# Kernel optimization log

Hardware: AMD Instinct MI355X
Metric: run time of the kernel (lower is better)

## Reference

```python
import jax, jax.numpy as jnp
import numpy as np

D_MODEL = 256
D_INNER = 512   # expand=2
D_STATE = 16
D_CONV = 4
DT_RANK = 16    # ceil(256/16)
N_LAYERS = 4
CITY = 300
BATCH = 32
EPS = 1e-5


def setup_inputs() -> dict:
    key = jax.random.key(0)
    ks = jax.random.split(key, 12)
    def rn(k, shape, scale=0.02):
        return (jax.random.normal(k, shape) * scale).astype(jnp.float32)
    inp = {}
    inp["coords"]   = jax.random.uniform(ks[0], (BATCH, CITY, 2), jnp.float32)
    inp["emb_W"]    = rn(ks[1], (D_MODEL, 2), 0.5)
    inp["emb_b"]    = jnp.zeros((D_MODEL,), jnp.float32)
    inp["ln_w"]     = jnp.ones((N_LAYERS, D_MODEL), jnp.float32)
    inp["ln_b"]     = jnp.zeros((N_LAYERS, D_MODEL), jnp.float32)
    inp["in_W"]     = rn(ks[2], (N_LAYERS, 2 * D_INNER, D_MODEL))
    inp["conv_W"]   = rn(ks[3], (N_LAYERS, D_INNER, D_CONV), 0.1)
    inp["conv_b"]   = jnp.zeros((N_LAYERS, D_INNER), jnp.float32)
    inp["xproj_W"]  = rn(ks[4], (N_LAYERS, DT_RANK + 2 * D_STATE, D_INNER))
    inp["dtproj_W"] = rn(ks[5], (N_LAYERS, D_INNER, DT_RANK), 0.1)
    inp["dtproj_b"] = rn(ks[6], (N_LAYERS, D_INNER), 0.1)
    # A initialized like mamba: S4D-real, A = -exp(A_log) with A in [1, 16]
    inp["A_log"]    = jnp.log(1.0 + jax.random.uniform(ks[7], (N_LAYERS, D_INNER, D_STATE), jnp.float32) * 15.0)
    inp["D_skip"]   = jnp.ones((N_LAYERS, D_INNER), jnp.float32)
    inp["out_W"]    = rn(ks[8], (N_LAYERS, D_MODEL, D_INNER))
    inp["normf_w"]  = jnp.ones((D_MODEL,), jnp.float32)
    inp["normf_b"]  = jnp.zeros((D_MODEL,), jnp.float32)
    inp["head_W"]   = rn(ks[9], (CITY, D_MODEL))
    return inp


def _layernorm(x, w, b):
    m = jnp.mean(x, axis=-1, keepdims=True)
    v = jnp.mean(jnp.square(x - m), axis=-1, keepdims=True)
    return (x - m) * jax.lax.rsqrt(v + EPS) * w + b


def _mamba_mixer(x, in_W, conv_W, conv_b, xproj_W, dtproj_W, dtproj_b, A_log, D_skip, out_W):
    # x: (B, L, d_model)
    Bsz = x.shape[0]
    xz = jnp.einsum('bld,ed->ble', x, in_W)            # (B, L, 2*d_inner)
    xi, z = jnp.split(xz, 2, axis=-1)                   # each (B, L, d_inner)
    # causal depthwise conv1d along L
    xc = jnp.swapaxes(xi, 1, 2)                         # (B, d_inner, L)
    xc = jax.lax.conv_general_dilated(
        xc, conv_W[:, None, :], (1,), [(D_CONV - 1, 0)],
        feature_group_count=D_INNER, dimension_numbers=('NCH', 'OIH', 'NCH'))
    xc = jax.nn.silu(jnp.swapaxes(xc, 1, 2) + conv_b)   # (B, L, d_inner)
    dbl = jnp.einsum('bld,ed->ble', xc, xproj_W)        # (B, L, dt_rank + 2*d_state)
    dt, Bm, Cm = jnp.split(dbl, [DT_RANK, DT_RANK + D_STATE], axis=-1)
    dt = jax.nn.softplus(jnp.einsum('blr,dr->bld', dt, dtproj_W) + dtproj_b)  # (B, L, d_inner)
    A = -jnp.exp(A_log)                                 # (d_inner, d_state)

    def step(h, inp):
        x_t, dt_t, B_t, C_t = inp                       # (B,dI),(B,dI),(B,dS),(B,dS)
        dA = jnp.exp(dt_t[..., None] * A)               # (B, dI, dS)
        h = dA * h + (dt_t * x_t)[..., None] * B_t[:, None, :]
        y = jnp.einsum('bds,bs->bd', h, C_t)
        return h, y

    h0 = jnp.zeros((Bsz, D_INNER, D_STATE), x.dtype)
    xs = (jnp.swapaxes(xc, 0, 1), jnp.swapaxes(dt, 0, 1),
          jnp.swapaxes(Bm, 0, 1), jnp.swapaxes(Cm, 0, 1))
    _, ys = jax.lax.scan(step, h0, xs)                  # ys: (L, B, d_inner)
    y = jnp.swapaxes(ys, 0, 1) + xc * D_skip
    y = y * jax.nn.silu(z)
    return jnp.einsum('ble,de->bld', y, out_W)          # (B, L, d_model)


def reference(coords, emb_W, emb_b, ln_w, ln_b, in_W, conv_W, conv_b, xproj_W,
              dtproj_W, dtproj_b, A_log, D_skip, out_W, normf_w, normf_b, head_W):
    x = jnp.einsum('blc,dc->bld', coords, emb_W) + emb_b
    residual = None
    for i in range(N_LAYERS):
        residual = x if residual is None else x + residual
        h = _layernorm(residual, ln_w[i], ln_b[i])
        x = _mamba_mixer(h, in_W[i], conv_W[i], conv_b[i], xproj_W[i],
                         dtproj_W[i], dtproj_b[i], A_log[i], D_skip[i], out_W[i])
    res = x + residual
    # final fused add + RMSNorm (is_rms_norm=True with LayerNorm weight/bias)
    rms = res * jax.lax.rsqrt(jnp.mean(res * res, axis=-1, keepdims=True) + EPS)
    out = rms * normf_w + normf_b
    logits = jnp.einsum('bld,cd->blc', out, head_W)     # (B, L, city_count)
    return logits
```

## Files before the change

kernel.cpp:

```cpp
#include <hip/hip_runtime.h>
#include <hip/hip_bf16.h>
#include <math.h>

#define D_MODEL 256
#define D_INNER 512
#define D_STATE 16
#define D_CONV 4
#define DT_RANK 16
#define N_LAYERS 4
#define CITY 300
#define BATCH 32
#define SEQ 300
#define NTOK (BATCH * SEQ)
#define NSEG 15
#define SEGLEN (SEQ / NSEG)

typedef __attribute__((ext_vector_type(8))) short short8v;
typedef __attribute__((ext_vector_type(4))) float f32x4;
typedef __attribute__((ext_vector_type(2))) float f32x2;

#define L2E_F 1.44269504088896340736f
#define LN2_F 0.69314718055994530942f

__device__ __forceinline__ float fexp2(float x) { return __builtin_amdgcn_exp2f(x); }
__device__ __forceinline__ float flog2(float x) { return __builtin_amdgcn_logf(x); }

__device__ __forceinline__ float fast_sig(float x) {
    return __builtin_amdgcn_rcpf(1.f + fexp2(-x * L2E_F));
}

__device__ __forceinline__ float softplus_f(float x) {
    float t = fexp2(-fabsf(x) * L2E_F);
    return fmaxf(x, 0.f) + flog2(1.f + t) * LN2_F;
}

__device__ __forceinline__ unsigned short f2b(float a) {
    __hip_bfloat16 h = __float2bfloat16(a);
    return *reinterpret_cast<unsigned short*>(&h);
}

__device__ __forceinline__ float b2f(unsigned short u) {
    unsigned int x = ((unsigned int)u) << 16;
    return __uint_as_float(x);
}

__device__ __forceinline__ float dtproj8(const float* rb, const f32x2* w2, float dtbv) {
    const f32x2* r2 = (const f32x2*)rb;
    f32x2 a0, a1, a2, a3;
    a0.x = dtbv; a0.y = 0.f;
    a1.x = 0.f; a1.y = 0.f;
    a2 = a1; a3 = a1;
    a0 = __builtin_elementwise_fma(r2[0], w2[0], a0);
    a1 = __builtin_elementwise_fma(r2[1], w2[1], a1);
    a2 = __builtin_elementwise_fma(r2[2], w2[2], a2);
    a3 = __builtin_elementwise_fma(r2[3], w2[3], a3);
    a0 = __builtin_elementwise_fma(r2[4], w2[4], a0);
    a1 = __builtin_elementwise_fma(r2[5], w2[5], a1);
    a2 = __builtin_elementwise_fma(r2[6], w2[6], a2);
    a3 = __builtin_elementwise_fma(r2[7], w2[7], a3);
    f32x2 s = (a0 + a1) + (a2 + a3);
    return s.x + s.y;
}

__global__ void cvt4_kernel(const float* __restrict__ s0, unsigned short* __restrict__ d0, int n0,
                            const float* __restrict__ s1, unsigned short* __restrict__ d1, int n1,
                            const float* __restrict__ s2, unsigned short* __restrict__ d2, int n2,
                            const float* __restrict__ s3, unsigned short* __restrict__ d3, int n3) {
    int stride = gridDim.x * blockDim.x;
    int tid = blockIdx.x * blockDim.x + threadIdx.x;
    for (int i = tid; i < n0 / 4; i += stride) {
        float4 v = ((const float4*)s0)[i];
        ushort4 o; o.x = f2b(v.x); o.y = f2b(v.y); o.z = f2b(v.z); o.w = f2b(v.w);
        ((ushort4*)d0)[i] = o;
    }
    for (int i = tid; i < n1 / 4; i += stride) {
        float4 v = ((const float4*)s1)[i];
        ushort4 o; o.x = f2b(v.x); o.y = f2b(v.y); o.z = f2b(v.z); o.w = f2b(v.w);
        ((ushort4*)d1)[i] = o;
    }
    for (int i = tid; i < n2 / 4; i += stride) {
        float4 v = ((const float4*)s2)[i];
        ushort4 o; o.x = f2b(v.x); o.y = f2b(v.y); o.z = f2b(v.z); o.w = f2b(v.w);
        ((ushort4*)d2)[i] = o;
    }
    for (int i = tid; i < n3 / 4; i += stride) {
        float4 v = ((const float4*)s3)[i];
        ushort4 o; o.x = f2b(v.x); o.y = f2b(v.y); o.z = f2b(v.z); o.w = f2b(v.w);
        ((ushort4*)d3)[i] = o;
    }
}

__global__ void embed_ln_kernel(const float* __restrict__ coords,
                                const float* __restrict__ eW,
                                const float* __restrict__ eb,
                                const float* __restrict__ w,
                                const float* __restrict__ b,
                                float* __restrict__ resid,
                                unsigned short* __restrict__ hb) {
    int t = blockIdx.x, d = threadIdx.x;
    float c0 = coords[t * 2 + 0];
    float c1 = coords[t * 2 + 1];
    float r = c0 * eW[d * 2 + 0] + c1 * eW[d * 2 + 1] + eb[d];
    resid[t * D_MODEL + d] = r;
    float s1 = r, s2 = r * r;
#pragma unroll
    for (int m = 1; m < 64; m <<= 1) {
        s1 += __shfl_xor(s1, m);
        s2 += __shfl_xor(s2, m);
    }
    __shared__ float p1[4], p2[4];
    if ((d & 63) == 0) { p1[d >> 6] = s1; p2[d >> 6] = s2; }
    __syncthreads();
    s1 = (p1[0] + p1[1]) + (p1[2] + p1[3]);
    s2 = (p2[0] + p2[1]) + (p2[2] + p2[3]);
    float mean = s1 * (1.f / D_MODEL);
    float var = s2 * (1.f / D_MODEL) - mean * mean;
    hb[t * D_MODEL + d] = f2b((r - mean) * rsqrtf(var + 1e-5f) * w[d] + b[d]);
}

template <int BM, int BN, bool GN, bool OB>
__global__ __launch_bounds__(256, 2) void gemm_mfma(const unsigned short* __restrict__ A,
                                                    const unsigned short* __restrict__ W,
                                                    void* __restrict__ C, int N, int K) {
    constexpr int TI = BM / 32;
    constexpr int TJ = BN / 32;
    __shared__ short Als[BM * 32];
    __shared__ short Bls[BN * 32];
    const int tid = threadIdx.x;
    const int lane = tid & 63, wid = tid >> 6;
    const int wr = wid >> 1, wc = wid & 1;
    const int t0 = blockIdx.x * BM, n0 = blockIdx.y * BN;
    f32x4 acc[TI][TJ] = {};

    for (int k0 = 0; k0 < K; k0 += 32) {
#pragma unroll
        for (int it = 0; it < BM / 64; ++it) {
            int s = tid + it * 256;
            int m = s >> 2, q = s & 3;
            uint4 p = *(const uint4*)(A + (size_t)(t0 + m) * K + k0 + q * 8);
            *(uint4*)&Als[(((m >> 4) * 4 + q) * 16 + (m & 15)) * 8] = p;
        }
#pragma unroll
        for (int it = 0; it < BN / 64; ++it) {
            int s = tid + it * 256;
            int n = s >> 2, q = s & 3;
            int nrow = n0 + n;
            uint4 p = make_uint4(0u, 0u, 0u, 0u);
            if (!GN || nrow < N)
                p = *(const uint4*)(W + (size_t)nrow * K + k0 + q * 8);
            *(uint4*)&Bls[(((n >> 4) * 4 + q) * 16 + (n & 15)) * 8] = p;
        }
        __syncthreads();
        short8v af[TI], bf[TJ];
#pragma unroll
        for (int i = 0; i < TI; i++)
            af[i] = *(const short8v*)&Als[(wr * TI + i) * 512 + lane * 8];
#pragma unroll
        for (int j = 0; j < TJ; j++)
            bf[j] = *(const short8v*)&Bls[(wc * TJ + j) * 512 + lane * 8];
#pragma unroll
        for (int i = 0; i < TI; i++)
#pragma unroll
            for (int j = 0; j < TJ; j++)
                acc[i][j] = __builtin_amdgcn_mfma_f32_16x16x32_bf16(
                    af[i], bf[j], acc[i][j], 0, 0, 0);
        __syncthreads();
    }
    const int rq = lane >> 4, cn = lane & 15;
#pragma unroll
    for (int i = 0; i < TI; i++) {
        int trow = t0 + wr * (BM / 2) + i * 16 + rq * 4;
#pragma unroll
        for (int j = 0; j < TJ; j++) {
            int ncol = n0 + wc * (BN / 2) + j * 16 + cn;
            if (!GN || ncol < N) {
#pragma unroll
                for (int reg = 0; reg < 4; reg++) {
                    if constexpr (OB)
                        ((unsigned short*)C)[(size_t)(trow + reg) * N + ncol] =
                            f2b(acc[i][j][reg]);
                    else
                        ((float*)C)[(size_t)(trow + reg) * N + ncol] = acc[i][j][reg];
                }
            }
        }
    }
}

template <bool RMS>
__global__ __launch_bounds__(256, 2) void gemm_out_ln(const unsigned short* __restrict__ A,
                                                      const unsigned short* __restrict__ W,
                                                      float* __restrict__ resid,
                                                      const float* __restrict__ w,
                                                      const float* __restrict__ b,
                                                      unsigned short* __restrict__ hb) {
    constexpr int TI = 2, TJ = 8;
    const int K = D_INNER;
    __shared__ short Als[64 * 32];
    __shared__ short Bls[256 * 32];
    __shared__ float rs1[2][64], rs2[2][64];
    const int tid = threadIdx.x;
    const int lane = tid & 63, wid = tid >> 6;
    const int wr = wid >> 1, wc = wid & 1;
    const int t0 = blockIdx.x * 64;
    f32x4 acc[TI][TJ] = {};

    for (int k0 = 0; k0 < K; k0 += 32) {
        {
            int s = tid;
            int m = s >> 2, q = s & 3;
            uint4 p = *(const uint4*)(A + (size_t)(t0 + m) * K + k0 + q * 8);
            *(uint4*)&Als[(((m >> 4) * 4 + q) * 16 + (m & 15)) * 8] = p;
        }
#pragma unroll
        for (int it = 0; it < 4; ++it) {
            int s = tid + it * 256;
            int n = s >> 2, q = s & 3;
            uint4 p = *(const uint4*)(W + (size_t)n * K + k0 + q * 8);
            *(uint4*)&Bls[(((n >> 4) * 4 + q) * 16 + (n & 15)) * 8] = p;
        }
        __syncthreads();
        short8v af[TI], bf[TJ];
#pragma unroll
        for (int i = 0; i < TI; i++)
            af[i] = *(const short8v*)&Als[(wr * TI + i) * 512 + lane * 8];
#pragma unroll
        for (int j = 0; j < TJ; j++)
            bf[j] = *(const short8v*)&Bls[(wc * TJ + j) * 512 + lane * 8];
#pragma unroll
        for (int i = 0; i < TI; i++)
#pragma unroll
            for (int j = 0; j < TJ; j++)
                acc[i][j] = __builtin_amdgcn_mfma_f32_16x16x32_bf16(
                    af[i], bf[j], acc[i][j], 0, 0, 0);
        __syncthreads();
    }
    const int rq = lane >> 4, cn = lane & 15;
    float s1p[TI][4], s2p[TI][4];
#pragma unroll
    for (int i = 0; i < TI; i++) {
        int trow = t0 + wr * 32 + i * 16 + rq * 4;
#pragma unroll
        for (int reg = 0; reg < 4; reg++) { s1p[i][reg] = 0.f; s2p[i][reg] = 0.f; }
#pragma unroll
        for (int j = 0; j < TJ; j++) {
            int c = wc * 128 + j * 16 + cn;
#pragma unroll
            for (int reg = 0; reg < 4; reg++) {
                float rv = acc[i][j][reg] + resid[(size_t)(trow + reg) * D_MODEL + c];
                acc[i][j][reg] = rv;
                s1p[i][reg] += rv;
                s2p[i][reg] = fmaf(rv, rv, s2p[i][reg]);
            }
        }
    }
#pragma unroll
    for (int m = 1; m < 16; m <<= 1) {
#pragma unroll
        for (int i = 0; i < TI; i++)
#pragma unroll
            for (int reg = 0; reg < 4; reg++) {
                s1p[i][reg] += __shfl_xor(s1p[i][reg], m);
                s2p[i][reg] += __shfl_xor(s2p[i][reg], m);
            }
    }
    if (cn == 0) {
#pragma unroll
        for (int i = 0; i < TI; i++)
#pragma unroll
            for (int reg = 0; reg < 4; reg++) {
                int rloc = wr * 32 + i * 16 + rq * 4 + reg;
                rs1[wc][rloc] = s1p[i][reg];
                rs2[wc][rloc] = s2p[i][reg];
            }
    }
    __syncthreads();
    float wv[TJ], bv[TJ];
#pragma unroll
    for (int j = 0; j < TJ; j++) {
        int c = wc * 128 + j * 16 + cn;
        wv[j] = w[c];
        bv[j] = b[c];
    }
#pragma unroll
    for (int i = 0; i < TI; i++) {
        int trow = t0 + wr * 32 + i * 16 + rq * 4;
#pragma unroll
        for (int reg = 0; reg < 4; reg++) {
            int rloc = wr * 32 + i * 16 + rq * 4 + reg;
            float S1 = rs1[0][rloc] + rs1[1][rloc];
            float S2 = rs2[0][rloc] + rs2[1][rloc];
            float mean, rstd;
            if constexpr (RMS) {
                mean = 0.f;
                rstd = rsqrtf(S2 * (1.f / D_MODEL) + 1e-5f);
            } else {
                mean = S1 * (1.f / D_MODEL);
                float var = S2 * (1.f / D_MODEL) - mean * mean;
                rstd = rsqrtf(var + 1e-5f);
            }
#pragma unroll
            for (int j = 0; j < TJ; j++) {
                int c = wc * 128 + j * 16 + cn;
                float rv = acc[i][j][reg];
                hb[(size_t)(trow + reg) * D_MODEL + c] =
                    f2b((rv - mean) * rstd * wv[j] + bv[j]);
                if constexpr (!RMS)
                    resid[(size_t)(trow + reg) * D_MODEL + c] = rv;
            }
        }
    }
}

__global__ void conv_silu_kernel(const unsigned short* __restrict__ xzb,
                                 const float* __restrict__ cW,
                                 const float* __restrict__ cb,
                                 unsigned short* __restrict__ xcb) {
    int idx = blockIdx.x * blockDim.x + threadIdx.x;
    int d4 = (idx & 127) * 4;
    int t = idx >> 7;
    int l = t % SEQ;
    float4 acc = *(const float4*)(cb + d4);
    float4 wA = *(const float4*)(cW + (d4 + 0) * 4);
    float4 wB = *(const float4*)(cW + (d4 + 1) * 4);
    float4 wC = *(const float4*)(cW + (d4 + 2) * 4);
    float4 wD = *(const float4*)(cW + (d4 + 3) * 4);
#pragma unroll
    for (int k = 0; k < D_CONV; k++) {
        int ll = l - 3 + k;
        if (ll >= 0) {
            ushort4 u = *(const ushort4*)(xzb + (size_t)(t - 3 + k) * 1024 + d4);
            float wa = (k == 0) ? wA.x : (k == 1) ? wA.y : (k == 2) ? wA.z : wA.w;
            float wb = (k == 0) ? wB.x : (k == 1) ? wB.y : (k == 2) ? wB.z : wB.w;
            float wc = (k == 0) ? wC.x : (k == 1) ? wC.y : (k == 2) ? wC.z : wC.w;
            float wd = (k == 0) ? wD.x : (k == 1) ? wD.y : (k == 2) ? wD.z : wD.w;
            acc.x = fmaf(b2f(u.x), wa, acc.x);
            acc.y = fmaf(b2f(u.y), wb, acc.y);
            acc.z = fmaf(b2f(u.z), wc, acc.z);
            acc.w = fmaf(b2f(u.w), wd, acc.w);
        }
    }
    ushort4 ob;
    ob.x = f2b(acc.x * fast_sig(acc.x));
    ob.y = f2b(acc.y * fast_sig(acc.y));
    ob.z = f2b(acc.z * fast_sig(acc.z));
    ob.w = f2b(acc.w * fast_sig(acc.w));
    *(ushort4*)(xcb + (size_t)t * 512 + d4) = ob;
}

__global__ __launch_bounds__(960) void scan_block(
    const unsigned short* __restrict__ xcb, const float* __restrict__ dbl,
    const unsigned short* __restrict__ xzb,
    const float* __restrict__ A_log, const float* __restrict__ Dskip,
    const float* __restrict__ dtW, const float* __restrict__ dtb,
    float* __restrict__ dts, unsigned short* __restrict__ yb) {
    __shared__ float lh[NSEG * D_STATE * 64];
    __shared__ float lsd[NSEG * 64];
    const int b = blockIdx.x, dg = blockIdx.y;
    const int tid = threadIdx.x;
    const int lane = tid & 63;
    const int seg = __builtin_amdgcn_readfirstlane(tid >> 6);
    const int d = (dg << 6) + lane;
    f32x2 A2[8], w2[8];
#pragma unroll
    for (int s4 = 0; s4 < 4; s4++) {
        float4 v = *(const float4*)(A_log + (size_t)d * D_STATE + s4 * 4);
        f32x2 pa, pb;
        pa.x = -fexp2(v.x * L2E_F) * L2E_F;
        pa.y = -fexp2(v.y * L2E_F) * L2E_F;
        pb.x = -fexp2(v.z * L2E_F) * L2E_F;
        pb.y = -fexp2(v.w * L2E_F) * L2E_F;
        A2[s4 * 2 + 0] = pa;
        A2[s4 * 2 + 1] = pb;
        float4 w = *(const float4*)(dtW + (size_t)d * DT_RANK + s4 * 4);
        f32x2 qa, qb;
        qa.x = w.x; qa.y = w.y;
        qb.x = w.z; qb.y = w.w;
        w2[s4 * 2 + 0] = qa;
        w2[s4 * 2 + 1] = qb;
    }
    const float dtbv = dtb[d], dsk = Dskip[d];
    const size_t tb = (size_t)b * SEQ + (size_t)seg * SEGLEN;
    const float* __restrict__ dr = dbl + tb * 48;
    const unsigned short* __restrict__ xp = xcb + tb * 512 + d;
    const unsigned short* __restrict__ zp = xzb + tb * 1024 + 512 + d;
    float* __restrict__ dtp = dts + tb * 512 + d;
    unsigned short* __restrict__ yp = yb + tb * 512 + d;

    {
        f32x2 h2[8];
#pragma unroll
        for (int i = 0; i < 8; i++) { h2[i].x = 0.f; h2[i].y = 0.f; }
        float sdt = 0.f;
        float dbA[32], dbB[32];
#pragma unroll
        for (int i = 0; i < 8; i++) ((float4*)dbA)[i] = ((const float4*)dr)[i];
        float xv = b2f(xp[0]);
        for (int l = 0; l < SEGLEN; l += 2) {
            const float4* nr1 = (const float4*)(dr + (size_t)(l + 1) * 48);
#pragma unroll
            for (int i = 0; i < 8; i++) ((float4*)dbB)[i] = nr1[i];
            float xv1 = b2f(xp[(size_t)(l + 1) * 512]);
            {
                float acc = dtproj8(dbA, w2, dtbv);
                float dtt = softplus_f(acc);
                dtp[(size_t)l * 512] = dtt;
                sdt += dtt;
                float dtx = dtt * xv;
                f32x2 dtt2, dtx2;
                dtt2.x = dtt; dtt2.y = dtt;
                dtx2.x = dtx; dtx2.y = dtx;
                const f32x2* B2 = (const f32x2*)(dbA + 16);
#pragma unroll
                for (int i = 0; i < 8; i++) {
                    f32x2 g = dtt2 * A2[i];
                    f32x2 e;
                    e.x = fexp2(g.x);
                    e.y = fexp2(g.y);
                    h2[i] = __builtin_elementwise_fma(e, h2[i], dtx2 * B2[i]);
                }
            }
            const float4* nr2 = (const float4*)(dr + (size_t)(l + 2) * 48);
#pragma unroll
            for (int i = 0; i < 8; i++) ((float4*)dbA)[i] = nr2[i];
            float xv2 = b2f(xp[(size_t)(l + 2) * 512]);
            if (l + 1 < SEGLEN) {
                float acc = dtproj8(dbB, w2, dtbv);
                float dtt = softplus_f(acc);
                dtp[(size_t)(l + 1) * 512] = dtt;
                sdt += dtt;
                float dtx = dtt * xv1;
                f32x2 dtt2, dtx2;
                dtt2.x = dtt; dtt2.y = dtt;
                dtx2.x = dtx; dtx2.y = dtx;
                const f32x2* B2 = (const f32x2*)(dbB + 16);
#pragma unroll
                for (int i = 0; i < 8; i++) {
                    f32x2 g = dtt2 * A2[i];
                    f32x2 e;
                    e.x = fexp2(g.x);
                    e.y = fexp2(g.y);
                    h2[i] = __builtin_elementwise_fma(e, h2[i], dtx2 * B2[i]);
                }
            }
            xv = xv2;
        }
#pragma unroll
        for (int i = 0; i < 8; i++) {
            lh[(seg * D_STATE + 2 * i + 0) * 64 + lane] = h2[i].x;
            lh[(seg * D_STATE + 2 * i + 1) * 64 + lane] = h2[i].y;
        }
        lsd[seg * 64 + lane] = sdt;
    }
    __syncthreads();
    for (int it = tid; it < D_STATE * 64; it += 960) {
        int ch = it & 63, s = it >> 6;
        float As2 = -fexp2(A_log[(size_t)((dg << 6) + ch) * D_STATE + s] * L2E_F) * L2E_F;
        float hl[NSEG], sd[NSEG];
#pragma unroll
        for (int sg = 0; sg < NSEG; sg++) {
            hl[sg] = lh[(sg * D_STATE + s) * 64 + ch];
            sd[sg] = lsd[sg * 64 + ch];
        }
        float H = 0.f;
#pragma unroll
        for (int sg = 0; sg < NSEG; sg++) {
            lh[(sg * D_STATE + s) * 64 + ch] = H;
            H = fmaf(fexp2(As2 * sd[sg]), H, hl[sg]);
        }
    }
    __syncthreads();
    {
        f32x2 h2[8];
#pragma unroll
        for (int i = 0; i < 8; i++) {
            h2[i].x = lh[(seg * D_STATE + 2 * i + 0) * 64 + lane];
            h2[i].y = lh[(seg * D_STATE + 2 * i + 1) * 64 + lane];
        }
        float dbA[32], dbB[32];
#pragma unroll
        for (int i = 0; i < 8; i++) ((float4*)dbA)[i] = ((const float4*)(dr + 16))[i];
        float xv = b2f(xp[0]), zv = b2f(zp[0]);
        float dt0 = dtp[0];
        for (int l = 0; l < SEGLEN; l += 2) {
            const float4* nr1 = (const float4*)(dr + (size_t)(l + 1) * 48 + 16);
#pragma unroll
            for (int i = 0; i < 8; i++) ((float4*)dbB)[i] = nr1[i];
            float xv1 = b2f(xp[(size_t)(l + 1) * 512]);
            float zv1 = b2f(zp[(size_t)(l + 1) * 1024]);
            float dt1 = dtp[(size_t)(l + 1) * 512];
            {
                float dtt = dt0;
                float dtx = dtt * xv;
                f32x2 dtt2, dtx2;
                dtt2.x = dtt; dtt2.y = dtt;
                dtx2.x = dtx; dtx2.y = dtx;
                f32x2 ya, yc;
                ya.x = 0.f; ya.y = 0.f; yc = ya;
                const f32x2* B2 = (const f32x2*)dbA;
                const f32x2* C2 = (const f32x2*)(dbA + 16);
#pragma unroll
                for (int i = 0; i < 8; i++) {
                    f32x2 g = dtt2 * A2[i];
                    f32x2 e;
                    e.x = fexp2(g.x);
                    e.y = fexp2(g.y);
                    h2[i] = __builtin_elementwise_fma(e, h2[i], dtx2 * B2[i]);
                    if (i & 1)
                        yc = __builtin_elementwise_fma(h2[i], C2[i], yc);
                    else
                        ya = __builtin_elementwise_fma(h2[i], C2[i], ya);
                }
                f32x2 ys = ya + yc;
                float y = ys.x + ys.y;
                yp[(size_t)l * 512] = f2b((y + xv * dsk) * (zv * fast_sig(zv)));
            }
            const float4* nr2 = (const float4*)(dr + (size_t)(l + 2) * 48 + 16);
#pragma unroll
            for (int i = 0; i < 8; i++) ((float4*)dbA)[i] = nr2[i];
            float xv2 = b2f(xp[(size_t)(l + 2) * 512]);
            float zv2 = b2f(zp[(size_t)(l + 2) * 1024]);
            float dt2 = dtp[(size_t)(l + 2) * 512];
            if (l + 1 < SEGLEN) {
                float dtt = dt1;
                float dtx = dtt * xv1;
                f32x2 dtt2, dtx2;
                dtt2.x = dtt; dtt2.y = dtt;
                dtx2.x = dtx; dtx2.y = dtx;
                f32x2 ya, yc;
                ya.x = 0.f; ya.y = 0.f; yc = ya;
                const f32x2* B2 = (const f32x2*)dbB;
                const f32x2* C2 = (const f32x2*)(dbB + 16);
#pragma unroll
                for (int i = 0; i < 8; i++) {
                    f32x2 g = dtt2 * A2[i];
                    f32x2 e;
                    e.x = fexp2(g.x);
                    e.y = fexp2(g.y);
                    h2[i] = __builtin_elementwise_fma(e, h2[i], dtx2 * B2[i]);
                    if (i & 1)
                        yc = __builtin_elementwise_fma(h2[i], C2[i], yc);
                    else
                        ya = __builtin_elementwise_fma(h2[i], C2[i], ya);
                }
                f32x2 ys = ya + yc;
                float y = ys.x + ys.y;
                yp[(size_t)(l + 1) * 512] = f2b((y + xv1 * dsk) * (zv1 * fast_sig(zv1)));
            }
            xv = xv2; zv = zv2; dt0 = dt2;
        }
    }
}

extern "C" void kernel_launch(void* const* d_in, const int* in_sizes, int n_in,
                              void* d_out, int out_size, void* d_ws, size_t ws_size,
                              hipStream_t stream) {
    const float* coords   = (const float*)d_in[0];
    const float* emb_W    = (const float*)d_in[1];
    const float* emb_b    = (const float*)d_in[2];
    const float* ln_w     = (const float*)d_in[3];
    const float* ln_b     = (const float*)d_in[4];
    const float* in_W     = (const float*)d_in[5];
    const float* conv_W   = (const float*)d_in[6];
    const float* conv_b   = (const float*)d_in[7];
    const float* xproj_W  = (const float*)d_in[8];
    const float* dtproj_W = (const float*)d_in[9];
    const float* dtproj_b = (const float*)d_in[10];
    const float* A_log    = (const float*)d_in[11];
    const float* D_skip   = (const float*)d_in[12];
    const float* out_W    = (const float*)d_in[13];
    const float* normf_w  = (const float*)d_in[14];
    const float* normf_b  = (const float*)d_in[15];
    const float* head_W   = (const float*)d_in[16];
    float* out = (float*)d_out;

    const int T = NTOK;
    float* resid = (float*)d_ws;
    float* dbl   = resid + (size_t)T * D_MODEL;
    float* dts   = dbl + (size_t)T * 48;
    unsigned short* hb     = (unsigned short*)(dts + (size_t)T * D_INNER);
    unsigned short* xzb    = hb + (size_t)T * D_MODEL;
    unsigned short* xcb    = xzb + (size_t)T * 2 * D_INNER;
    unsigned short* yb     = xcb + (size_t)T * D_INNER;
    unsigned short* wb_in  = yb + (size_t)T * D_INNER;
    unsigned short* wb_xp  = wb_in + (size_t)N_LAYERS * 2 * D_INNER * D_MODEL;
    unsigned short* wb_out = wb_xp + (size_t)N_LAYERS * 48 * D_INNER;
    unsigned short* wb_hd  = wb_out + (size_t)N_LAYERS * D_MODEL * D_INNER;

    cvt4_kernel<<<256, 256, 0, stream>>>(
        in_W, wb_in, N_LAYERS * 2 * D_INNER * D_MODEL,
        xproj_W, wb_xp, N_LAYERS * 48 * D_INNER,
        out_W, wb_out, N_LAYERS * D_MODEL * D_INNER,
        head_W, wb_hd, CITY * D_MODEL);

    embed_ln_kernel<<<T, D_MODEL, 0, stream>>>(coords, emb_W, emb_b, ln_w, ln_b, resid, hb);

    for (int i = 0; i < N_LAYERS; i++) {
        gemm_mfma<128, 128, false, true><<<dim3(T / 128, 8), 256, 0, stream>>>(
            hb, wb_in + (size_t)i * 2 * D_INNER * D_MODEL, xzb, 2 * D_INNER, D_MODEL);
        conv_silu_kernel<<<T * 128 / 256, 256, 0, stream>>>(
            xzb, conv_W + i * D_INNER * D_CONV, conv_b + i * D_INNER, xcb);
        gemm_mfma<64, 64, true, false><<<dim3(T / 64, 1), 256, 0, stream>>>(
            xcb, wb_xp + (size_t)i * 48 * D_INNER, dbl, 48, D_INNER);
        scan_block<<<dim3(BATCH, 8), 960, 0, stream>>>(
            xcb, dbl, xzb, A_log + (size_t)i * D_INNER * D_STATE, D_skip + i * D_INNER,
            dtproj_W + (size_t)i * D_INNER * DT_RANK, dtproj_b + i * D_INNER, dts, yb);
        if (i < N_LAYERS - 1)
            gemm_out_ln<false><<<T / 64, 256, 0, stream>>>(
                yb, wb_out + (size_t)i * D_MODEL * D_INNER, resid,
                ln_w + (i + 1) * D_MODEL, ln_b + (i + 1) * D_MODEL, hb);
        else
            gemm_out_ln<true><<<T / 64, 256, 0, stream>>>(
                yb, wb_out + (size_t)i * D_MODEL * D_INNER, resid,
                normf_w, normf_b, hb);
    }

    gemm_mfma<64, 64, true, false><<<dim3(T / 64, 5), 256, 0, stream>>>(
        hb, wb_hd, out, CITY, D_MODEL);
}
```

Measured before the change: 493.2 us.

## Split scan blocks into 32-channel groups with 512-thread blocks

Restructures the chunked selective scan so each block handles 32 channels instead of 64. Blocks now have 512 threads (16 segment slots, with one idle wave slot clamped to the last segment), and the grid grows to 32x16 blocks. The cross-segment carry pass now maps exactly one thread per (channel, state) pair. The intent is more blocks and better CU occupancy on the latency-bound scan. The cost is that 32-lane channel groups fill only half of each 64-wide wavefront, which loses coalescing width, and one of the 16 waves idles outside the carry pass.

```diff
diff --git a/kernel.cpp b/kernel.cpp
--- a/kernel.cpp
+++ b/kernel.cpp
@@ -14,6 +14,7 @@
 #define NTOK (BATCH * SEQ)
 #define NSEG 15
 #define SEGLEN (SEQ / NSEG)
+#define CPB 32
 
 typedef __attribute__((ext_vector_type(8))) short short8v;
 typedef __attribute__((ext_vector_type(4))) float f32x4;
@@ -348,19 +349,19 @@
     *(ushort4*)(xcb + (size_t)t * 512 + d4) = ob;
 }
 
-__global__ __launch_bounds__(960) void scan_block(
+__global__ __launch_bounds__(512) void scan_block(
     const unsigned short* __restrict__ xcb, const float* __restrict__ dbl,
     const unsigned short* __restrict__ xzb,
     const float* __restrict__ A_log, const float* __restrict__ Dskip,
     const float* __restrict__ dtW, const float* __restrict__ dtb,
     float* __restrict__ dts, unsigned short* __restrict__ yb) {
-    __shared__ float lh[NSEG * D_STATE * 64];
-    __shared__ float lsd[NSEG * 64];
+    __shared__ float lh[NSEG * D_STATE * CPB];
+    __shared__ float lsd[NSEG * CPB];
     const int b = blockIdx.x, dg = blockIdx.y;
     const int tid = threadIdx.x;
-    const int lane = tid & 63;
-    const int seg = __builtin_amdgcn_readfirstlane(tid >> 6);
-    const int d = (dg << 6) + lane;
+    const int ch = tid & (CPB - 1);
+    const int seg = tid >> 5;
+    const int d = dg * CPB + ch;
     f32x2 A2[8], w2[8];
 #pragma unroll
     for (int s4 = 0; s4 < 4; s4++) {
@@ -380,14 +381,15 @@
         w2[s4 * 2 + 1] = qb;
     }
     const float dtbv = dtb[d], dsk = Dskip[d];
-    const size_t tb = (size_t)b * SEQ + (size_t)seg * SEGLEN;
+    const int segc = (seg < NSEG) ? seg : (NSEG - 1);
+    const size_t tb = (size_t)b * SEQ + (size_t)segc * SEGLEN;
     const float* __restrict__ dr = dbl + tb * 48;
     const unsigned short* __restrict__ xp = xcb + tb * 512 + d;
     const unsigned short* __restrict__ zp = xzb + tb * 1024 + 512 + d;
     float* __restrict__ dtp = dts + tb * 512 + d;
     unsigned short* __restrict__ yp = yb + tb * 512 + d;
 
-    {
+    if (seg < NSEG) {
         f32x2 h2[8];
 #pragma unroll
         for (int i = 0; i < 8; i++) { h2[i].x = 0.f; h2[i].y = 0.f; }
@@ -447,35 +449,36 @@
         }
 #pragma unroll
         for (int i = 0; i < 8; i++) {
-            lh[(seg * D_STATE + 2 * i + 0) * 64 + lane] = h2[i].x;
-            lh[(seg * D_STATE + 2 * i + 1) * 64 + lane] = h2[i].y;
-        }
-        lsd[seg * 64 + lane] = sdt;
-    }
-    __syncthreads();
-    for (int it = tid; it < D_STATE * 64; it += 960) {
-        int ch = it & 63, s = it >> 6;
-        float As2 = -fexp2(A_log[(size_t)((dg << 6) + ch) * D_STATE + s] * L2E_F) * L2E_F;
-        float hl[NSEG], sd[NSEG];
-#pragma unroll
-        for (int sg = 0; sg < NSEG; sg++) {
-            hl[sg] = lh[(sg * D_STATE + s) * 64 + ch];
-            sd[sg] = lsd[sg * 64 + ch];
-        }
-        float H = 0.f;
-#pragma unroll
-        for (int sg = 0; sg < NSEG; sg++) {
-            lh[(sg * D_STATE + s) * 64 + ch] = H;
-            H = fmaf(fexp2(As2 * sd[sg]), H, hl[sg]);
-        }
+            lh[(seg * D_STATE + 2 * i + 0) * CPB + ch] = h2[i].x;
+            lh[(seg * D_STATE + 2 * i + 1) * CPB + ch] = h2[i].y;
+        }
+        lsd[seg * CPB + ch] = sdt;
     }
     __syncthreads();
     {
+        int it = tid;
+        int c2 = it & (CPB - 1), s = it >> 5;
+        float As2 = -fexp2(A_log[(size_t)(dg * CPB + c2) * D_STATE + s] * L2E_F) * L2E_F;
+        float hl[NSEG], sd[NSEG];
+#pragma unroll
+        for (int sg = 0; sg < NSEG; sg++) {
+            hl[sg] = lh[(sg * D_STATE + s) * CPB + c2];
+            sd[sg] = lsd[sg * CPB + c2];
+        }
+        float H = 0.f;
+#pragma unroll
+        for (int sg = 0; sg < NSEG; sg++) {
+            lh[(sg * D_STATE + s) * CPB + c2] = H;
+            H = fmaf(fexp2(As2 * sd[sg]), H, hl[sg]);
+        }
+    }
+    __syncthreads();
+    if (seg < NSEG) {
         f32x2 h2[8];
 #pragma unroll
         for (int i = 0; i < 8; i++) {
-            h2[i].x = lh[(seg * D_STATE + 2 * i + 0) * 64 + lane];
-            h2[i].y = lh[(seg * D_STATE + 2 * i + 1) * 64 + lane];
+            h2[i].x = lh[(seg * D_STATE + 2 * i + 0) * CPB + ch];
+            h2[i].y = lh[(seg * D_STATE + 2 * i + 1) * CPB + ch];
         }
         float dbA[32], dbB[32];
 #pragma unroll
@@ -602,7 +605,7 @@
             xzb, conv_W + i * D_INNER * D_CONV, conv_b + i * D_INNER, xcb);
         gemm_mfma<64, 64, true, false><<<dim3(T / 64, 1), 256, 0, stream>>>(
             xcb, wb_xp + (size_t)i * 48 * D_INNER, dbl, 48, D_INNER);
-        scan_block<<<dim3(BATCH, 8), 960, 0, stream>>>(
+        scan_block<<<dim3(BATCH, D_INNER / CPB), 512, 0, stream>>>(
             xcb, dbl, xzb, A_log + (size_t)i * D_INNER * D_STATE, D_skip + i * D_INNER,
             dtproj_W + (size_t)i * D_INNER * DT_RANK, dtproj_b + i * D_INNER, dts, yb);
         if (i < N_LAYERS - 1)
```

New measurement: 551.0 us. 11.7% more time.
